# Performance work log

Measured on AMD Instinct MI355X. Metric: run time of the kernel, lower is better.

Reference implementation:

```python
import jax, jax.numpy as jnp
import numpy as np

NUM_POINTS = 2_000_000
N = 2_000_000

# SH constants (standard real spherical harmonics, as in gaussian-splatting)
C0 = 0.28209479177387814
C1 = 0.4886025119029199
C2 = (1.0925484305920792, -1.0925484305920792, 0.31539156525252005,
      -1.0925484305920792, 0.5462742152960396)
C3 = (-0.5900435899266435, 2.890611442640554, -0.4570457994644658,
      0.3731763325901154, -0.4570457994644658, 1.445305721320277,
      -0.5900435899266435)


def sh_basis_deg3(dirs):
    # dirs: [N,3] unit vectors -> basis [N,16]
    x, y, z = dirs[:, 0], dirs[:, 1], dirs[:, 2]
    xx, yy, zz = x * x, y * y, z * z
    xy, yz, xz = x * y, y * z, x * z
    one = jnp.ones_like(x)
    return jnp.stack([
        C0 * one,
        -C1 * y, C1 * z, -C1 * x,
        C2[0] * xy, C2[1] * yz, C2[2] * (2.0 * zz - xx - yy),
        C2[3] * xz, C2[4] * (xx - yy),
        C3[0] * y * (3.0 * xx - yy), C3[1] * xy * z,
        C3[2] * y * (4.0 * zz - xx - yy),
        C3[3] * z * (2.0 * zz - 3.0 * xx - 3.0 * yy),
        C3[4] * x * (4.0 * zz - xx - yy),
        C3[5] * z * (xx - yy), C3[6] * x * (xx - yy),
    ], axis=-1)


def setup_inputs() -> dict:
    key = jax.random.key(0)
    ks = jax.random.split(key, 8)
    return {
        "positions": jax.random.normal(ks[0], (N, 3), jnp.float32),
        "indexes": jax.random.randint(ks[1], (N,), 0, NUM_POINTS, jnp.int64)
            if jax.config.jax_enable_x64 else
            jax.random.randint(ks[1], (N,), 0, NUM_POINTS, jnp.int32),
        "cam_pos": jax.random.normal(ks[2], (3,), jnp.float32),
        "glo_feature": jax.random.normal(ks[3], (1, 16), jnp.float32),
        "base_sh": jax.random.normal(ks[4], (NUM_POINTS, 3, 1), jnp.float32),
        "higher_sh": jnp.zeros((NUM_POINTS, 3, 15), jnp.float32)
            + 0.01 * jax.random.normal(ks[5], (NUM_POINTS, 3, 15), jnp.float32),
        "w1": jax.random.normal(ks[6], (16, 32), jnp.float32) * (1.0 / np.sqrt(16)),
        "b1": jnp.zeros((32,), jnp.float32),
        "ln_w": jnp.ones((32,), jnp.float32),
        "ln_b": jnp.zeros((32,), jnp.float32),
        "w2": jax.random.normal(ks[7], (32, 12), jnp.float32) * (1.0 / np.sqrt(32)),
        "b2": jnp.zeros((12,), jnp.float32),
    }


def mlp(glo, w1, b1, ln_w, ln_b, w2, b2, out_scale=1e-12):
    h = glo @ w1 + b1                      # [1,32]
    mu = jnp.mean(h, axis=-1, keepdims=True)
    var = jnp.mean((h - mu) ** 2, axis=-1, keepdims=True)
    h = (h - mu) * jax.lax.rsqrt(var + 1e-5) * ln_w + ln_b
    h = jax.nn.relu(h)
    return (h @ w2 + b2) * out_scale       # [1,12]


def reference(positions, indexes, cam_pos, glo_feature, base_sh, higher_sh,
              w1, b1, ln_w, ln_b, w2, b2):
    sh_features = jnp.concatenate([base_sh, higher_sh], axis=2)  # [P,3,16]
    sh = sh_features[indexes]                                    # gather [N,3,16]
    dirs = positions - cam_pos
    dirs = dirs / jnp.linalg.norm(dirs, axis=-1, keepdims=True)
    basis = sh_basis_deg3(dirs)                                  # [N,16]
    colors = jnp.einsum('nck,nk->nc', sh, basis) + 0.5           # [N,3]
    colors4 = jnp.concatenate([colors, jnp.ones_like(colors[:, :1])], axis=1)  # [N,4]
    affine_res = mlp(glo_feature, w1, b1, ln_w, ln_b, w2, b2).reshape(1, 3, 4)
    affine = affine_res + jnp.eye(3, 4, dtype=jnp.float32)[None]  # [1,3,4]
    out = jnp.einsum('nj,ij->ni', colors4, affine[0])             # [N,3]
    return jnp.clip(out, 0.0, 1.0), jnp.mean(jnp.abs(affine_res))
```

## Files before the change

### kernel.cpp

```cpp
#include <hip/hip_runtime.h>
#include <math.h>


__global__ __launch_bounds__(256) void transfer_sh_fused(
    const float* __restrict__ positions,
    const int*   __restrict__ indexes,
    const float* __restrict__ cam_pos,
    const float* __restrict__ glo,
    const float* __restrict__ base_sh,
    const float* __restrict__ higher_sh,
    const float* __restrict__ w1,
    const float* __restrict__ b1,
    const float* __restrict__ ln_w,
    const float* __restrict__ ln_b,
    const float* __restrict__ w2,
    const float* __restrict__ b2,
    float* __restrict__ out,
    float* __restrict__ mean_out,
    int n)
{
    __shared__ float aff[12];
    __shared__ float hsh[32];
    __shared__ float ssh[12];

    const int t = threadIdx.x;
    const int i = blockIdx.x * 256 + t;
    const bool active = (i < n);
    const int ie = active ? i : (n - 1);

    unsigned idx = (unsigned)__builtin_nontemporal_load(indexes + ie);

    float px = __builtin_nontemporal_load(positions + 3 * ie + 0);
    float py = __builtin_nontemporal_load(positions + 3 * ie + 1);
    float pz = __builtin_nontemporal_load(positions + 3 * ie + 2);

    float a0 = base_sh[3 * idx + 0];
    float a1 = base_sh[3 * idx + 1];
    float a2 = base_sh[3 * idx + 2];

    unsigned fo = 45u * idx;
    const float4* W = (const float4*)(higher_sh + (fo & ~3u));
    float4 v[12];
    #pragma unroll
    for (int q = 0; q < 12; ++q) v[q] = W[q];

    if (t < 64) {
        float h = 0.f;
        if (t < 32) {
            h = b1[t];
            #pragma unroll
            for (int k = 0; k < 16; ++k) h += glo[k] * w1[k * 32 + t];
        }
        float s = h;
        #pragma unroll
        for (int off = 32; off > 0; off >>= 1) s += __shfl_down(s, off);
        float mu = __shfl(s, 0) * (1.f / 32.f);
        float d = (t < 32) ? (h - mu) : 0.f;
        float v2 = d * d;
        #pragma unroll
        for (int off = 32; off > 0; off >>= 1) v2 += __shfl_down(v2, off);
        float var = __shfl(v2, 0) * (1.f / 32.f);
        float inv = rsqrtf(var + 1e-5f);
        if (t < 32) {
            float hv = (h - mu) * inv * ln_w[t] + ln_b[t];
            hsh[t] = hv > 0.f ? hv : 0.f;
        }
    }
    __syncthreads();
    if (t < 12) {
        float s2 = b2[t];
        #pragma unroll
        for (int j = 0; j < 32; ++j) s2 += hsh[j] * w2[j * 12 + t];
        s2 *= 1e-12f;
        ssh[t] = fabsf(s2);
        float e = ((t & 3) == (t >> 2)) ? 1.f : 0.f;
        aff[t] = s2 + e;
    }
    __syncthreads();
    if (blockIdx.x == 0 && t == 0) {
        float sa = 0.f;
        #pragma unroll
        for (int q2 = 0; q2 < 12; ++q2) sa += ssh[q2];
        *mean_out = sa * (1.f / 12.f);
    }

    float dx = px - cam_pos[0];
    float dy = py - cam_pos[1];
    float dz = pz - cam_pos[2];
    float rn = rsqrtf(dx * dx + dy * dy + dz * dz);
    float x = dx * rn, y = dy * rn, z = dz * rn;

    float xx = x * x, yy = y * y, zz = z * z;
    float xy = x * y, yz = y * z, xz = x * z;

    float b[16];
    b[1]  = -0.4886025119029199f * y;
    b[2]  =  0.4886025119029199f * z;
    b[3]  = -0.4886025119029199f * x;
    b[4]  =  1.0925484305920792f * xy;
    b[5]  = -1.0925484305920792f * yz;
    b[6]  =  0.31539156525252005f * (2.f * zz - xx - yy);
    b[7]  = -1.0925484305920792f * xz;
    b[8]  =  0.5462742152960396f * (xx - yy);
    b[9]  = -0.5900435899266435f * y * (3.f * xx - yy);
    b[10] =  2.890611442640554f  * xy * z;
    b[11] = -0.4570457994644658f * y * (4.f * zz - xx - yy);
    b[12] =  0.3731763325901154f * z * (2.f * zz - 3.f * xx - 3.f * yy);
    b[13] = -0.4570457994644658f * x * (4.f * zz - xx - yy);
    b[14] =  1.445305721320277f  * z * (xx - yy);
    b[15] = -0.5900435899266435f * x * (xx - yy);

    const float C0 = 0.28209479177387814f;
    float c0 = a0 * C0 + 0.5f;
    float c1 = a1 * C0 + 0.5f;
    float c2 = a2 * C0 + 0.5f;

    float Wf[48];
    #pragma unroll
    for (int q = 0; q < 12; ++q) {
        Wf[4 * q + 0] = v[q].x; Wf[4 * q + 1] = v[q].y;
        Wf[4 * q + 2] = v[q].z; Wf[4 * q + 3] = v[q].w;
    }

#define ACC(M)                                      \
    {                                               \
        _Pragma("unroll")                           \
        for (int k = 0; k < 15; ++k) {              \
            c0 += Wf[(M) + k]      * b[k + 1];      \
            c1 += Wf[(M) + 15 + k] * b[k + 1];      \
            c2 += Wf[(M) + 30 + k] * b[k + 1];      \
        }                                           \
    }
    switch (fo & 3u) {
        case 0: ACC(0) break;
        case 1: ACC(1) break;
        case 2: ACC(2) break;
        default: ACC(3) break;
    }
#undef ACC

    if (active) {
        #pragma unroll
        for (int r = 0; r < 3; ++r) {
            float vv = c0 * aff[4 * r + 0] + c1 * aff[4 * r + 1] +
                       c2 * aff[4 * r + 2] + aff[4 * r + 3];
            vv = fminf(fmaxf(vv, 0.f), 1.f);
            __builtin_nontemporal_store(vv, out + 3 * i + r);
        }
    }
}

extern "C" void kernel_launch(void* const* d_in, const int* in_sizes, int n_in,
                              void* d_out, int out_size, void* d_ws, size_t ws_size,
                              hipStream_t stream) {
    const float* positions = (const float*)d_in[0];
    const int*   indexes   = (const int*)d_in[1];
    const float* cam_pos   = (const float*)d_in[2];
    const float* glo       = (const float*)d_in[3];
    const float* base_sh   = (const float*)d_in[4];
    const float* higher_sh = (const float*)d_in[5];
    const float* w1        = (const float*)d_in[6];
    const float* b1        = (const float*)d_in[7];
    const float* ln_w      = (const float*)d_in[8];
    const float* ln_b      = (const float*)d_in[9];
    const float* w2        = (const float*)d_in[10];
    const float* b2        = (const float*)d_in[11];

    float* out = (float*)d_out;

    int n = in_sizes[0] / 3;
    float* mean_out = out + (out_size - 1);

    int block = 256;
    int grid = (n + block - 1) / block;
    transfer_sh_fused<<<grid, block, 0, stream>>>(
        positions, indexes, cam_pos, glo, base_sh, higher_sh,
        w1, b1, ln_w, ln_b, w2, b2, out, mean_out, n);
}
```

Measured before the change: 569.5 us.

## Bucket-sort point indices to localize SH gathers, with XCD-aware block remap

Adds a coarse 256-bin counting sort of the gather indices (histogram, scan, scatter into a permutation) and a new main kernel that walks points in bucket order. Neighbouring threads then gather nearby rows of higher_sh/base_sh, which should improve L2/MALL locality. Block IDs are also remapped so each XCD handles a contiguous range of buckets. In exchange it adds four extra launches, atomics, and an extra pass over the indices, and the positions loads and output stores become scattered. The old fused kernel is kept as a fallback when the workspace is too small.

```diff
diff --git a/kernel.cpp b/kernel.cpp
--- a/kernel.cpp
+++ b/kernel.cpp
@@ -1,6 +1,248 @@
 #include <hip/hip_runtime.h>
 #include <math.h>
 
+
+#define NB 256
+
+__global__ __launch_bounds__(512) void zero_kernel(unsigned* __restrict__ p)
+{
+    p[threadIdx.x] = 0u;
+}
+
+__global__ __launch_bounds__(256) void hist_kernel(
+    const int* __restrict__ idx, unsigned* __restrict__ hist,
+    float scale, int n)
+{
+    __shared__ unsigned lh[NB];
+    const int t = threadIdx.x;
+    lh[t] = 0u;
+    __syncthreads();
+    for (long e = (long)blockIdx.x * 256 + t; e < n; e += (long)gridDim.x * 256) {
+        unsigned b = (unsigned)(idx[e] * scale);
+        if (b > NB - 1u) b = NB - 1u;
+        atomicAdd(&lh[b], 1u);
+    }
+    __syncthreads();
+    unsigned c = lh[t];
+    if (c) atomicAdd(&hist[t], c);
+}
+
+__global__ __launch_bounds__(64) void scan_kernel(
+    const unsigned* __restrict__ hist, unsigned* __restrict__ cursors)
+{
+    const int t = threadIdx.x;
+    unsigned v0 = hist[4 * t + 0], v1 = hist[4 * t + 1];
+    unsigned v2 = hist[4 * t + 2], v3 = hist[4 * t + 3];
+    unsigned s4 = v0 + v1 + v2 + v3;
+    unsigned s = s4;
+    #pragma unroll
+    for (int off = 1; off < 64; off <<= 1) {
+        unsigned x = __shfl_up(s, off);
+        if (t >= off) s += x;
+    }
+    unsigned base = s - s4;
+    cursors[4 * t + 0] = base; base += v0;
+    cursors[4 * t + 1] = base; base += v1;
+    cursors[4 * t + 2] = base; base += v2;
+    cursors[4 * t + 3] = base;
+}
+
+#define SC_ELEMS 16
+__global__ __launch_bounds__(256) void scatter_kernel(
+    const int* __restrict__ idx, unsigned* __restrict__ cursors,
+    int* __restrict__ perm, float scale, int n)
+{
+    __shared__ unsigned lhist[NB];
+    __shared__ unsigned lbase[NB];
+    const int t = threadIdx.x;
+    const long base0 = (long)blockIdx.x * (256L * SC_ELEMS);
+
+    lhist[t] = 0u;
+    __syncthreads();
+
+    unsigned mybin[SC_ELEMS];
+    #pragma unroll
+    for (int k = 0; k < SC_ELEMS; ++k) {
+        long e = base0 + (long)k * 256 + t;
+        unsigned b = 0xFFFFFFFFu;
+        if (e < n) {
+            b = (unsigned)(idx[e] * scale);
+            if (b > NB - 1u) b = NB - 1u;
+            atomicAdd(&lhist[b], 1u);
+        }
+        mybin[k] = b;
+    }
+    __syncthreads();
+    unsigned c = lhist[t];
+    if (c) lbase[t] = atomicAdd(&cursors[t], c);
+    lhist[t] = 0u;
+    __syncthreads();
+    #pragma unroll
+    for (int k = 0; k < SC_ELEMS; ++k) {
+        unsigned b = mybin[k];
+        if (b != 0xFFFFFFFFu) {
+            unsigned r = atomicAdd(&lhist[b], 1u);
+            perm[lbase[b] + r] = (int)(base0 + (long)k * 256 + t);
+        }
+    }
+}
+
+__global__ __launch_bounds__(256) void transfer_sh_perm(
+    const float* __restrict__ positions,
+    const int*   __restrict__ indexes,
+    const int*   __restrict__ perm,
+    const float* __restrict__ cam_pos,
+    const float* __restrict__ glo,
+    const float* __restrict__ base_sh,
+    const float* __restrict__ higher_sh,
+    const float* __restrict__ w1,
+    const float* __restrict__ b1,
+    const float* __restrict__ ln_w,
+    const float* __restrict__ ln_b,
+    const float* __restrict__ w2,
+    const float* __restrict__ b2,
+    float* __restrict__ out,
+    float* __restrict__ mean_out,
+    int n)
+{
+    __shared__ float aff[12];
+    __shared__ float hsh[32];
+    __shared__ float ssh[12];
+
+    const int t = threadIdx.x;
+
+    const unsigned nwg = gridDim.x;
+    const unsigned q = nwg >> 3, r = nwg & 7u;
+    const unsigned xcd = blockIdx.x & 7u, pos = blockIdx.x >> 3;
+    const unsigned wg = (xcd < r ? xcd * (q + 1u)
+                                 : r * (q + 1u) + (xcd - r) * q) + pos;
+
+    const int j = (int)wg * 256 + t;
+    const bool active = (j < n);
+    const int je = active ? j : (n - 1);
+    const int i = perm[je];
+
+    unsigned idx = (unsigned)indexes[i];
+
+    float px = positions[3 * i + 0];
+    float py = positions[3 * i + 1];
+    float pz = positions[3 * i + 2];
+
+    float a0 = base_sh[3 * idx + 0];
+    float a1 = base_sh[3 * idx + 1];
+    float a2 = base_sh[3 * idx + 2];
+
+    unsigned fo = 45u * idx;
+    const float4* W = (const float4*)(higher_sh + (fo & ~3u));
+    float4 v[12];
+    #pragma unroll
+    for (int qq = 0; qq < 12; ++qq) v[qq] = W[qq];
+
+    if (t < 64) {
+        float h = 0.f;
+        if (t < 32) {
+            h = b1[t];
+            #pragma unroll
+            for (int k = 0; k < 16; ++k) h += glo[k] * w1[k * 32 + t];
+        }
+        float s = h;
+        #pragma unroll
+        for (int off = 32; off > 0; off >>= 1) s += __shfl_down(s, off);
+        float mu = __shfl(s, 0) * (1.f / 32.f);
+        float d = (t < 32) ? (h - mu) : 0.f;
+        float v2 = d * d;
+        #pragma unroll
+        for (int off = 32; off > 0; off >>= 1) v2 += __shfl_down(v2, off);
+        float var = __shfl(v2, 0) * (1.f / 32.f);
+        float inv = rsqrtf(var + 1e-5f);
+        if (t < 32) {
+            float hv = (h - mu) * inv * ln_w[t] + ln_b[t];
+            hsh[t] = hv > 0.f ? hv : 0.f;
+        }
+    }
+    __syncthreads();
+    if (t < 12) {
+        float s2 = b2[t];
+        #pragma unroll
+        for (int jj = 0; jj < 32; ++jj) s2 += hsh[jj] * w2[jj * 12 + t];
+        s2 *= 1e-12f;
+        ssh[t] = fabsf(s2);
+        float e = ((t & 3) == (t >> 2)) ? 1.f : 0.f;
+        aff[t] = s2 + e;
+    }
+    __syncthreads();
+    if (blockIdx.x == 0 && t == 0) {
+        float sa = 0.f;
+        #pragma unroll
+        for (int q2 = 0; q2 < 12; ++q2) sa += ssh[q2];
+        *mean_out = sa * (1.f / 12.f);
+    }
+
+    float dx = px - cam_pos[0];
+    float dy = py - cam_pos[1];
+    float dz = pz - cam_pos[2];
+    float rn = rsqrtf(dx * dx + dy * dy + dz * dz);
+    float x = dx * rn, y = dy * rn, z = dz * rn;
+
+    float xx = x * x, yy = y * y, zz = z * z;
+    float xy = x * y, yz = y * z, xz = x * z;
+
+    float b[16];
+    b[1]  = -0.4886025119029199f * y;
+    b[2]  =  0.4886025119029199f * z;
+    b[3]  = -0.4886025119029199f * x;
+    b[4]  =  1.0925484305920792f * xy;
+    b[5]  = -1.0925484305920792f * yz;
+    b[6]  =  0.31539156525252005f * (2.f * zz - xx - yy);
+    b[7]  = -1.0925484305920792f * xz;
+    b[8]  =  0.5462742152960396f * (xx - yy);
+    b[9]  = -0.5900435899266435f * y * (3.f * xx - yy);
+    b[10] =  2.890611442640554f  * xy * z;
+    b[11] = -0.4570457994644658f * y * (4.f * zz - xx - yy);
+    b[12] =  0.3731763325901154f * z * (2.f * zz - 3.f * xx - 3.f * yy);
+    b[13] = -0.4570457994644658f * x * (4.f * zz - xx - yy);
+    b[14] =  1.445305721320277f  * z * (xx - yy);
+    b[15] = -0.5900435899266435f * x * (xx - yy);
+
+    const float C0 = 0.28209479177387814f;
+    float c0 = a0 * C0 + 0.5f;
+    float c1 = a1 * C0 + 0.5f;
+    float c2 = a2 * C0 + 0.5f;
+
+    float Wf[48];
+    #pragma unroll
+    for (int qq = 0; qq < 12; ++qq) {
+        Wf[4 * qq + 0] = v[qq].x; Wf[4 * qq + 1] = v[qq].y;
+        Wf[4 * qq + 2] = v[qq].z; Wf[4 * qq + 3] = v[qq].w;
+    }
+
+#define ACC(M)                                      \
+    {                                               \
+        _Pragma("unroll")                           \
+        for (int k = 0; k < 15; ++k) {              \
+            c0 += Wf[(M) + k]      * b[k + 1];      \
+            c1 += Wf[(M) + 15 + k] * b[k + 1];      \
+            c2 += Wf[(M) + 30 + k] * b[k + 1];      \
+        }                                           \
+    }
+    switch (fo & 3u) {
+        case 0: ACC(0) break;
+        case 1: ACC(1) break;
+        case 2: ACC(2) break;
+        default: ACC(3) break;
+    }
+#undef ACC
+
+    if (active) {
+        #pragma unroll
+        for (int rr = 0; rr < 3; ++rr) {
+            float vv = c0 * aff[4 * rr + 0] + c1 * aff[4 * rr + 1] +
+                       c2 * aff[4 * rr + 2] + aff[4 * rr + 3];
+            vv = fminf(fmaxf(vv, 0.f), 1.f);
+            out[3 * i + rr] = vv;
+        }
+    }
+}
 
 __global__ __launch_bounds__(256) void transfer_sh_fused(
     const float* __restrict__ positions,
@@ -29,11 +271,9 @@
     const int ie = active ? i : (n - 1);
 
     unsigned idx = (unsigned)__builtin_nontemporal_load(indexes + ie);
-
     float px = __builtin_nontemporal_load(positions + 3 * ie + 0);
     float py = __builtin_nontemporal_load(positions + 3 * ie + 1);
     float pz = __builtin_nontemporal_load(positions + 3 * ie + 2);
-
     float a0 = base_sh[3 * idx + 0];
     float a1 = base_sh[3 * idx + 1];
     float a2 = base_sh[3 * idx + 2];
@@ -42,7 +282,7 @@
     const float4* W = (const float4*)(higher_sh + (fo & ~3u));
     float4 v[12];
     #pragma unroll
-    for (int q = 0; q < 12; ++q) v[q] = W[q];
+    for (int qq = 0; qq < 12; ++qq) v[qq] = W[qq];
 
     if (t < 64) {
         float h = 0.f;
@@ -70,7 +310,7 @@
     if (t < 12) {
         float s2 = b2[t];
         #pragma unroll
-        for (int j = 0; j < 32; ++j) s2 += hsh[j] * w2[j * 12 + t];
+        for (int jj = 0; jj < 32; ++jj) s2 += hsh[jj] * w2[jj * 12 + t];
         s2 *= 1e-12f;
         ssh[t] = fabsf(s2);
         float e = ((t & 3) == (t >> 2)) ? 1.f : 0.f;
@@ -89,7 +329,6 @@
     float dz = pz - cam_pos[2];
     float rn = rsqrtf(dx * dx + dy * dy + dz * dz);
     float x = dx * rn, y = dy * rn, z = dz * rn;
-
     float xx = x * x, yy = y * y, zz = z * z;
     float xy = x * y, yz = y * z, xz = x * z;
 
@@ -117,9 +356,9 @@
 
     float Wf[48];
     #pragma unroll
-    for (int q = 0; q < 12; ++q) {
-        Wf[4 * q + 0] = v[q].x; Wf[4 * q + 1] = v[q].y;
-        Wf[4 * q + 2] = v[q].z; Wf[4 * q + 3] = v[q].w;
+    for (int qq = 0; qq < 12; ++qq) {
+        Wf[4 * qq + 0] = v[qq].x; Wf[4 * qq + 1] = v[qq].y;
+        Wf[4 * qq + 2] = v[qq].z; Wf[4 * qq + 3] = v[qq].w;
     }
 
 #define ACC(M)                                      \
@@ -141,11 +380,11 @@
 
     if (active) {
         #pragma unroll
-        for (int r = 0; r < 3; ++r) {
-            float vv = c0 * aff[4 * r + 0] + c1 * aff[4 * r + 1] +
-                       c2 * aff[4 * r + 2] + aff[4 * r + 3];
+        for (int rr = 0; rr < 3; ++rr) {
+            float vv = c0 * aff[4 * rr + 0] + c1 * aff[4 * rr + 1] +
+                       c2 * aff[4 * rr + 2] + aff[4 * rr + 3];
             vv = fminf(fmaxf(vv, 0.f), 1.f);
-            __builtin_nontemporal_store(vv, out + 3 * i + r);
+            __builtin_nontemporal_store(vv, out + 3 * i + rr);
         }
     }
 }
@@ -167,13 +406,32 @@
     const float* b2        = (const float*)d_in[11];
 
     float* out = (float*)d_out;
-
     int n = in_sizes[0] / 3;
+    int P = in_sizes[4] / 3;
     float* mean_out = out + (out_size - 1);
 
+    size_t need = (size_t)(2 * NB + n) * sizeof(int);
     int block = 256;
     int grid = (n + block - 1) / block;
-    transfer_sh_fused<<<grid, block, 0, stream>>>(
-        positions, indexes, cam_pos, glo, base_sh, higher_sh,
-        w1, b1, ln_w, ln_b, w2, b2, out, mean_out, n);
-}
+
+    if (ws_size >= need && P > 0) {
+        unsigned* hist    = (unsigned*)d_ws;
+        unsigned* cursors = hist + NB;
+        int*      perm    = (int*)(hist + 2 * NB);
+        float scale = (float)NB / (float)P;
+
+        zero_kernel<<<1, 512, 0, stream>>>(hist);
+        hist_kernel<<<2048, 256, 0, stream>>>(indexes, hist, scale, n);
+        scan_kernel<<<1, 64, 0, stream>>>(hist, cursors);
+        int sgrid = (n + 256 * SC_ELEMS - 1) / (256 * SC_ELEMS);
+        scatter_kernel<<<sgrid, 256, 0, stream>>>(indexes, cursors, perm,
+                                                  scale, n);
+        transfer_sh_perm<<<grid, block, 0, stream>>>(
+            positions, indexes, perm, cam_pos, glo, base_sh, higher_sh,
+            w1, b1, ln_w, ln_b, w2, b2, out, mean_out, n);
+    } else {
+        transfer_sh_fused<<<grid, block, 0, stream>>>(
+            positions, indexes, cam_pos, glo, base_sh, higher_sh,
+            w1, b1, ln_w, ln_b, w2, b2, out, mean_out, n);
+    }
+}
```

Measured after the change: 690.0 us. +21.2%, slower.
